# Kernel tuning notes

Hardware: AMD Instinct MI355X
Metric: run time of the kernel (lower is better)

The kernel has to match this reference:

```python
import jax, jax.numpy as jnp
import numpy as np

B, L, D_MODEL = 2, 2048, 1024
D_INNER, D_STATE, DT_RANK, D_CONV = 2048, 16, 64, 4
EPS = 1e-5


def setup_inputs() -> dict:
    key = jax.random.key(0)
    ks = jax.random.split(key, 12)
    s = lambda fan: 1.0 / np.sqrt(fan)
    return {
        "x": jax.random.normal(ks[0], (B, L, D_MODEL), jnp.float32),
        "norm_w": jnp.ones((D_MODEL,), jnp.float32),
        "W_in": jax.random.normal(ks[1], (2 * D_INNER, D_MODEL), jnp.float32) * s(D_MODEL),
        "W_conv": jax.random.normal(ks[2], (D_INNER, D_CONV), jnp.float32) * s(D_CONV),
        "b_conv": jnp.zeros((D_INNER,), jnp.float32),
        "W_xproj": jax.random.normal(ks[3], (DT_RANK + 2 * D_STATE, D_INNER), jnp.float32) * s(D_INNER),
        "W_dt": jax.random.normal(ks[4], (D_INNER, DT_RANK), jnp.float32) * s(DT_RANK),
        "b_dt": jax.random.normal(ks[5], (D_INNER,), jnp.float32) * 0.1,
        # A initialized as log(1..d_state) per channel (standard Mamba S4D-real init)
        "A_log": jnp.log(jnp.broadcast_to(jnp.arange(1, D_STATE + 1, dtype=jnp.float32), (D_INNER, D_STATE))),
        "D": jnp.ones((D_INNER,), jnp.float32),
        "W_out": jax.random.normal(ks[6], (D_MODEL, D_INNER), jnp.float32) * s(D_INNER),
    }


def _mamba_residual(x, norm_w, W_in, W_conv, b_conv, W_xproj, W_dt, b_dt, A_log, D, W_out):
    # RMSNorm
    xn = x * jax.lax.rsqrt(jnp.mean(x * x, axis=-1, keepdims=True) + EPS) * norm_w
    # in_proj -> split into u (ssm branch) and z (gate)
    xz = jnp.einsum("bld,ed->ble", xn, W_in)            # [b, l, 2*d_inner]
    u, z = jnp.split(xz, 2, axis=-1)                     # each [b, l, d_inner]
    # depthwise causal conv1d over time
    u_t = jnp.transpose(u, (0, 2, 1))                    # [b, d_inner, l]
    u_c = jax.lax.conv_general_dilated(
        u_t, W_conv[:, None, :], window_strides=(1,),
        padding=[(D_CONV - 1, 0)], feature_group_count=D_INNER,
        dimension_numbers=("NCH", "OIH", "NCH"))
    u_c = jax.nn.silu(u_c + b_conv[None, :, None])       # [b, d_inner, l]
    u = jnp.transpose(u_c, (0, 2, 1))                    # [b, l, d_inner]
    # x_proj -> (dt, B, C)
    x_dbl = jnp.einsum("bld,ed->ble", u, W_xproj)        # [b, l, dt_rank+2n]
    dt, Bm, Cm = jnp.split(x_dbl, [DT_RANK, DT_RANK + D_STATE], axis=-1)
    dt = jax.nn.softplus(jnp.einsum("blr,dr->bld", dt, W_dt) + b_dt)  # [b, l, d_inner]
    A = -jnp.exp(A_log)                                  # [d_inner, n]

    # selective scan over time
    def step(h, ins):
        dt_t, B_t, C_t, u_t = ins                        # [b,d],[b,n],[b,n],[b,d]
        dA = jnp.exp(dt_t[..., None] * A)                # [b, d, n]
        h = dA * h + (dt_t * u_t)[..., None] * B_t[:, None, :]
        y = jnp.einsum("bdn,bn->bd", h, C_t)
        return h, y

    h0 = jnp.zeros((x.shape[0], D_INNER, D_STATE), x.dtype)
    ins = (jnp.transpose(dt, (1, 0, 2)), jnp.transpose(Bm, (1, 0, 2)),
           jnp.transpose(Cm, (1, 0, 2)), jnp.transpose(u, (1, 0, 2)))
    _, ys = jax.lax.scan(step, h0, ins)                  # [l, b, d_inner]
    y = jnp.transpose(ys, (1, 0, 2)) + u * D             # [b, l, d_inner]
    y = y * jax.nn.silu(z)
    out = jnp.einsum("ble,de->bld", y, W_out)
    return out + x  # residual (block_mode 'residual'/'none')


def reference(x, norm_w, W_in, W_conv, b_conv, W_xproj, W_dt, b_dt, A_log, D, W_out):
    return _mamba_residual(x, norm_w, W_in, W_conv, b_conv, W_xproj, W_dt, b_dt, A_log, D, W_out)
```

## Files before the change

### kernel.cpp

```cpp
#include <hip/hip_runtime.h>

typedef unsigned short u16;
typedef unsigned int u32;
typedef short bf16x8 __attribute__((ext_vector_type(8)));
typedef float f32x4 __attribute__((ext_vector_type(4)));

static constexpr int LS = 2048;
static constexpr int DM = 1024;
static constexpr int DI = 2048;
static constexpr int DSn = 16;
static constexpr int DTRk = 64;
static constexpr int MR = 4096;
static constexpr int NCH = 64;
static constexpr int CL = LS / NCH;
static constexpr float L2E = 1.44269504f;

#define DEV __device__ __forceinline__

DEV u16 f2bf(float f) {
  u32 u = __float_as_uint(f);
  u32 r = (u + 0x7FFF + ((u >> 16) & 1)) >> 16;
  return (u16)r;
}
DEV float bf2f(u16 h) { return __uint_as_float(((u32)h) << 16); }

DEV void gload16(const u16* g, u16* l) {
  __builtin_amdgcn_global_load_lds((const __attribute__((address_space(1))) u32*)g,
                                   (__attribute__((address_space(3))) u32*)l, 16, 0, 0);
}

DEV void bar() { asm volatile("s_barrier" ::: "memory"); }

#define CALC_POWERS(dst, basev)                                              \
  do {                                                                       \
    const float e1_ = (basev);                                               \
    const float e2_ = e1_ * e1_, e3_ = e2_ * e1_, e4_ = e2_ * e2_;           \
    const float e5_ = e4_ * e1_, e6_ = e4_ * e2_, e7_ = e4_ * e3_,           \
                e8_ = e4_ * e4_;                                             \
    dst[0] = e1_; dst[1] = e2_; dst[2] = e3_; dst[3] = e4_;                  \
    dst[4] = e5_; dst[5] = e6_; dst[6] = e7_; dst[7] = e8_;                  \
    dst[8] = e8_ * e1_;  dst[9] = e8_ * e2_;  dst[10] = e8_ * e3_;           \
    dst[11] = e8_ * e4_; dst[12] = e8_ * e5_; dst[13] = e8_ * e6_;           \
    dst[14] = e8_ * e7_; dst[15] = e8_ * e8_;                                \
  } while (0)

__global__ __launch_bounds__(256) void cvt_weights(const float* __restrict__ W_in,
                                                   const float* __restrict__ W_out,
                                                   const float* __restrict__ W_dt,
                                                   const float* __restrict__ W_xp,
                                                   u16* __restrict__ Win_b,
                                                   u16* __restrict__ Wout_b,
                                                   u16* __restrict__ Wdt_b,
                                                   u16* __restrict__ Wxp_b) {
  const int N0 = 4096 * 1024;
  const int N1 = N0 + 1024 * 2048;
  const int N2 = N1 + 2048 * 64;
  const int N3 = N2 + 128 * 2048;
  int i = blockIdx.x * 256 + threadIdx.x;
  const int stride = gridDim.x * 256;
  for (; i < N3; i += stride) {
    if (i < N0) {
      Win_b[i] = f2bf(W_in[i]);
    } else if (i < N1) {
      const int j = i - N0; Wout_b[j] = f2bf(W_out[j]);
    } else if (i < N2) {
      const int j = i - N1; Wdt_b[j] = f2bf(W_dt[j]);
    } else {
      const int j = i - N2; const int r = j >> 11, c = j & 2047;
      Wxp_b[j] = (r < 96) ? f2bf(W_xp[r * 2048 + c]) : (u16)0;
    }
  }
}

__global__ __launch_bounds__(256) void rmsnorm_kernel(const float* __restrict__ x,
                                                      const float* __restrict__ w,
                                                      u16* __restrict__ xn) {
  const int row = blockIdx.x;
  const int tid = threadIdx.x;
  const float4 v = reinterpret_cast<const float4*>(x + (size_t)row * DM)[tid];
  float ss = v.x * v.x + v.y * v.y + v.z * v.z + v.w * v.w;
#pragma unroll
  for (int o = 32; o; o >>= 1) ss += __shfl_xor(ss, o);
  __shared__ float red[4];
  if ((tid & 63) == 0) red[tid >> 6] = ss;
  __syncthreads();
  const float tot = red[0] + red[1] + red[2] + red[3];
  const float scale = rsqrtf(tot * (1.0f / DM) + 1e-5f);
  const float4 wv = reinterpret_cast<const float4*>(w)[tid];
  ushort4 o4;
  o4.x = f2bf(v.x * scale * wv.x);
  o4.y = f2bf(v.y * scale * wv.y);
  o4.z = f2bf(v.z * scale * wv.z);
  o4.w = f2bf(v.w * scale * wv.w);
  *reinterpret_cast<ushort4*>(&xn[(size_t)row * DM + tid * 4]) = o4;
}

template <int EPI>
__global__ __launch_bounds__(512, 4) void gemm128n256(const u16* __restrict__ A,
                                                      const u16* __restrict__ Bw,
                                                      int M, int N, int K, int Klen,
                                                      u16* __restrict__ outB,
                                                      float* __restrict__ outF) {
  __shared__ __align__(16) u16 SL[2 * 12288];
  const int tid = threadIdx.x;
  const int lane = tid & 63;
  const int wid = tid >> 6;
  const int wr = wid >> 2;
  const int wc = wid & 3;
  const int lrow = lane & 15;
  const int kq = lane >> 4;

  const int nwg = gridDim.x * gridDim.y;
  int wg = blockIdx.y * gridDim.x + blockIdx.x;
  wg = (wg & 7) * (nwg >> 3) + (wg >> 3);
  const int bn = (wg % gridDim.x) * 256;
  const int bm = (wg / gridDim.x) * 128;
  const int koff = blockIdx.z * Klen;

  const int nt = Klen >> 5;

  f32x4 acc[4][4] = {};
  bf16x8 a[4], b[4];

  const int srA = tid >> 2;
  const int slA = (tid & 3) ^ ((srA >> 1) & 3);
  const int srB0 = tid >> 2, srB1 = 128 + (tid >> 2);
  const int slB0 = (tid & 3) ^ ((srB0 >> 1) & 3);
  const int slB1 = (tid & 3) ^ ((srB1 >> 1) & 3);

#define STAGE_TILE(ktile, sup)                                                          \
  do {                                                                                  \
    const int k0_ = koff + (ktile) * 32;                                                \
    gload16(A + (size_t)(bm + srA) * K + k0_ + slA * 8, &SL[(sup) + tid * 8]);          \
    gload16(Bw + (size_t)(bn + srB0) * K + k0_ + slB0 * 8, &SL[(sup) + 4096 + tid * 8]);\
    gload16(Bw + (size_t)(bn + srB1) * K + k0_ + slB1 * 8, &SL[(sup) + 8192 + tid * 8]);\
  } while (0)

  STAGE_TILE(0, 0);
  asm volatile("s_waitcnt vmcnt(0)" ::: "memory");
  bar();

  for (int t = 0; t < nt; ++t) {
    const int cs = (t & 1) * 12288;
    const int ns = ((t + 1) & 1) * 12288;
    if (t + 1 < nt) STAGE_TILE(t + 1, ns);
#pragma unroll
    for (int m = 0; m < 4; ++m) {
      const int row = wr * 64 + m * 16 + lrow;
      a[m] = *reinterpret_cast<const bf16x8*>(
          &SL[cs + row * 32 + (kq ^ ((row >> 1) & 3)) * 8]);
    }
#pragma unroll
    for (int n = 0; n < 4; ++n) {
      const int row = wc * 64 + n * 16 + lrow;
      b[n] = *reinterpret_cast<const bf16x8*>(
          &SL[cs + 4096 + row * 32 + (kq ^ ((row >> 1) & 3)) * 8]);
    }
    __builtin_amdgcn_s_setprio(1);
#pragma unroll
    for (int m = 0; m < 4; ++m)
#pragma unroll
      for (int n = 0; n < 4; ++n)
        acc[m][n] = __builtin_amdgcn_mfma_f32_16x16x32_bf16(a[m], b[n], acc[m][n], 0, 0, 0);
    __builtin_amdgcn_s_setprio(0);
    if (t + 1 < nt) {
      asm volatile("s_waitcnt vmcnt(0)" ::: "memory");
      bar();
    }
  }
#undef STAGE_TILE

  if (EPI == 0) {
#pragma unroll
    for (int m = 0; m < 4; ++m)
#pragma unroll
      for (int n = 0; n < 4; ++n) {
        const int col = bn + wc * 64 + n * 16 + lrow;
#pragma unroll
        for (int rr = 0; rr < 4; ++rr) {
          const int row = bm + wr * 64 + m * 16 + kq * 4 + rr;
          outB[(size_t)row * N + col] = f2bf(acc[m][n][rr]);
        }
      }
  } else {
    float* dstF = outF + (size_t)blockIdx.z * MR * N;
#pragma unroll
    for (int m = 0; m < 4; ++m)
#pragma unroll
      for (int n = 0; n < 4; ++n) {
        const int col = bn + wc * 64 + n * 16 + lrow;
#pragma unroll
        for (int rr = 0; rr < 4; ++rr) {
          const int row = bm + wr * 64 + m * 16 + kq * 4 + rr;
          dstF[(size_t)row * N + col] = acc[m][n][rr];
        }
      }
  }
}

__global__ __launch_bounds__(256) void outproj_reduce4(const float* __restrict__ p,
                                                       const float* __restrict__ x,
                                                       float* __restrict__ out) {
  const int id = blockIdx.x * 256 + threadIdx.x;
  float4 o = reinterpret_cast<const float4*>(x)[id];
#pragma unroll
  for (int s = 0; s < 4; ++s) {
    const float4 a = reinterpret_cast<const float4*>(p + (size_t)s * MR * 1024)[id];
    o.x += a.x; o.y += a.y; o.z += a.z; o.w += a.w;
  }
  reinterpret_cast<float4*>(out)[id] = o;
}

__global__ __launch_bounds__(256) void gemm_dt(const u16* __restrict__ A,
                                               const u16* __restrict__ Bw,
                                               int M, int N, int K,
                                               u16* __restrict__ outB,
                                               const float* __restrict__ aux) {
  __shared__ __align__(16) u16 As[128 * 32];
  __shared__ __align__(16) u16 Bs[128 * 32];
  const int tid = threadIdx.x;
  const int lane = tid & 63;
  const int wid = tid >> 6;
  const int wr = wid >> 1, wc = wid & 1;
  const int nwg = gridDim.x * gridDim.y;
  int wg = blockIdx.y * gridDim.x + blockIdx.x;
  wg = (wg & 7) * (nwg >> 3) + (wg >> 3);
  const int bn = (wg % gridDim.x) * 128;
  const int bm = (wg / gridDim.x) * 128;
  const int r0 = tid >> 2;
  const int c0 = (tid & 3) * 8;
  const int lrow = lane & 15, kq = lane >> 4;

  f32x4 acc[4][4] = {};

  const u16* Ab = A + (size_t)bm * K;
  const u16* Bb = Bw + (size_t)bn * K;

  for (int k0 = 0; k0 < K; k0 += 32) {
    gload16(Ab + (size_t)r0 * K + k0 + c0, &As[r0 * 32 + c0]);
    gload16(Ab + (size_t)(r0 + 64) * K + k0 + c0, &As[(r0 + 64) * 32 + c0]);
    gload16(Bb + (size_t)r0 * K + k0 + c0, &Bs[r0 * 32 + c0]);
    gload16(Bb + (size_t)(r0 + 64) * K + k0 + c0, &Bs[(r0 + 64) * 32 + c0]);
    __syncthreads();
    bf16x8 af[4], bfr[4];
#pragma unroll
    for (int m = 0; m < 4; ++m)
      af[m] = *reinterpret_cast<const bf16x8*>(&As[(wr * 64 + m * 16 + lrow) * 32 + kq * 8]);
#pragma unroll
    for (int n = 0; n < 4; ++n)
      bfr[n] = *reinterpret_cast<const bf16x8*>(&Bs[(wc * 64 + n * 16 + lrow) * 32 + kq * 8]);
#pragma unroll
    for (int m = 0; m < 4; ++m)
#pragma unroll
      for (int n = 0; n < 4; ++n)
        acc[m][n] = __builtin_amdgcn_mfma_f32_16x16x32_bf16(af[m], bfr[n], acc[m][n], 0, 0, 0);
    __syncthreads();
  }

#pragma unroll
  for (int m = 0; m < 4; ++m) {
#pragma unroll
    for (int n = 0; n < 4; ++n) {
      const int col = bn + wc * 64 + n * 16 + lrow;
#pragma unroll
      for (int r = 0; r < 4; ++r) {
        const int row = bm + wr * 64 + m * 16 + kq * 4 + r;
        const float xv = acc[m][n][r] + aux[col];
        const float sp = fmaxf(xv, 0.f) + log1pf(__expf(-fabsf(xv)));
        outB[(size_t)row * N + col] = f2bf(sp);
      }
    }
  }
}

__global__ __launch_bounds__(256) void gemm_xproj_splitk(const u16* __restrict__ A,
                                                         const u16* __restrict__ Bw,
                                                         float* __restrict__ p0,
                                                         float* __restrict__ p1) {
  __shared__ __align__(16) u16 As[128 * 32];
  __shared__ __align__(16) u16 Bs[128 * 32];
  const int tid = threadIdx.x;
  const int lane = tid & 63;
  const int wid = tid >> 6;
  const int wr = wid >> 1, wc = wid & 1;
  const int kp = blockIdx.x;
  const int bm = blockIdx.y * 128;
  const int koff = kp * 256;
  const int r0 = tid >> 2;
  const int c0 = (tid & 3) * 8;
  const int lrow = lane & 15, kq = lane >> 4;

  f32x4 acc[4][4] = {};
  const u16* Ab = A + (size_t)bm * DI + koff;
  const u16* Bb = Bw + koff;

  for (int k0 = 0; k0 < 256; k0 += 32) {
    gload16(Ab + (size_t)r0 * DI + k0 + c0, &As[r0 * 32 + c0]);
    gload16(Ab + (size_t)(r0 + 64) * DI + k0 + c0, &As[(r0 + 64) * 32 + c0]);
    gload16(Bb + (size_t)r0 * DI + k0 + c0, &Bs[r0 * 32 + c0]);
    gload16(Bb + (size_t)(r0 + 64) * DI + k0 + c0, &Bs[(r0 + 64) * 32 + c0]);
    __syncthreads();
    bf16x8 af[4], bfr[4];
#pragma unroll
    for (int m = 0; m < 4; ++m)
      af[m] = *reinterpret_cast<const bf16x8*>(&As[(wr * 64 + m * 16 + lrow) * 32 + kq * 8]);
#pragma unroll
    for (int n = 0; n < 4; ++n)
      bfr[n] = *reinterpret_cast<const bf16x8*>(&Bs[(wc * 64 + n * 16 + lrow) * 32 + kq * 8]);
#pragma unroll
    for (int m = 0; m < 4; ++m)
#pragma unroll
      for (int n = 0; n < 4; ++n)
        acc[m][n] = __builtin_amdgcn_mfma_f32_16x16x32_bf16(af[m], bfr[n], acc[m][n], 0, 0, 0);
    __syncthreads();
  }

  float* dst = (kp < 4 ? p0 : p1) + (size_t)(kp & 3) * MR * 128;
#pragma unroll
  for (int m = 0; m < 4; ++m)
#pragma unroll
    for (int n = 0; n < 4; ++n) {
      const int col = wc * 64 + n * 16 + lrow;
#pragma unroll
      for (int r = 0; r < 4; ++r) {
        const int row = bm + wr * 64 + m * 16 + kq * 4 + r;
        dst[(size_t)row * 128 + col] = acc[m][n][r];
      }
    }
}

__global__ __launch_bounds__(256) void xproj_reduce(const float* __restrict__ p0,
                                                    const float* __restrict__ p1,
                                                    float* __restrict__ xdbl,
                                                    u16* __restrict__ dtr) {
  const int id = blockIdx.x * 256 + threadIdx.x;
  const int row = id >> 7, col = id & 127;
  float s = 0.f;
#pragma unroll
  for (int kp = 0; kp < 4; ++kp) s += p0[(size_t)kp * MR * 128 + id];
#pragma unroll
  for (int kp = 0; kp < 4; ++kp) s += p1[(size_t)kp * MR * 128 + id];
  if (col < 96) xdbl[(size_t)row * 96 + col] = s;
  if (col < 64) dtr[(size_t)row * 64 + col] = f2bf(s);
}

__global__ __launch_bounds__(256) void conv_silu_kernel(const u16* __restrict__ xz,
                                                        const float* __restrict__ Wc,
                                                        const float* __restrict__ bc,
                                                        u16* __restrict__ uc) {
  const int id = blockIdx.x * 256 + threadIdx.x;
  const int d8 = id & (DI / 8 - 1);
  const int t = (id >> 8) & (LS - 1);
  const int b = id >> 19;
  const int d0 = d8 * 8;
  const size_t rowb = (size_t)b * LS;
  bf16x8 r[4];
#pragma unroll
  for (int k = 0; k < 4; ++k) {
    const int tt = t - 3 + k;
    if (tt >= 0)
      r[k] = *reinterpret_cast<const bf16x8*>(&xz[(rowb + tt) * (2 * DI) + d0]);
    else
      r[k] = bf16x8{0, 0, 0, 0, 0, 0, 0, 0};
  }
  const float4 bc0 = *reinterpret_cast<const float4*>(&bc[d0]);
  const float4 bc1 = *reinterpret_cast<const float4*>(&bc[d0 + 4]);
  const float bcv[8] = {bc0.x, bc0.y, bc0.z, bc0.w, bc1.x, bc1.y, bc1.z, bc1.w};
  u16 o[8];
#pragma unroll
  for (int j = 0; j < 8; ++j) {
    const float4 w = *reinterpret_cast<const float4*>(&Wc[(d0 + j) * 4]);
    float s = bcv[j];
    s += bf2f((u16)r[0][j]) * w.x;
    s += bf2f((u16)r[1][j]) * w.y;
    s += bf2f((u16)r[2][j]) * w.z;
    s += bf2f((u16)r[3][j]) * w.w;
    const float sl = s / (1.f + __expf(-s));
    o[j] = f2bf(sl);
  }
  *reinterpret_cast<bf16x8*>(&uc[(rowb + t) * DI + d0]) =
      *reinterpret_cast<const bf16x8*>(o);
}


__global__ __launch_bounds__(128, 4) void scan_phase1(const u16* __restrict__ dtb,
                                                      const float* __restrict__ xdbl,
                                                      const u16* __restrict__ uc,
                                                      const float* __restrict__ Alog,
                                                      float* __restrict__ P,
                                                      float* __restrict__ S) {
  __shared__ __align__(16) u16 s_dt[16 * 128];
  __shared__ __align__(16) u16 s_uc[16 * 128];
  __shared__ __align__(16) float s_b[16 * 16];
  const int tid = threadIdx.x;
  const int blk = blockIdx.x;
  const int d0 = (blk & 15) * 128;
  const int c = (blk >> 4) & (NCH - 1);
  const int b = blk >> 10;
  const int d = d0 + tid;
  const size_t tbase = (size_t)b * LS + c * CL;

  float Av[16];
  bool fastA = true;
#pragma unroll
  for (int j = 0; j < 16; j += 4) {
    const float4 Alv = *reinterpret_cast<const float4*>(&Alog[d * DSn + j]);
    Av[j + 0] = -__expf(Alv.x); Av[j + 1] = -__expf(Alv.y);
    Av[j + 2] = -__expf(Alv.z); Av[j + 3] = -__expf(Alv.w);
  }
#pragma unroll
  for (int j = 0; j < 16; ++j)
    fastA = fastA && (fabsf(Av[j] + (float)(j + 1)) < 1e-3f * (float)(j + 1));

  float h[16];
#pragma unroll
  for (int j = 0; j < 16; ++j) h[j] = 0.f;
  float sdt = 0.f;

  for (int w = 0; w < 2; ++w) {
    const size_t twb = tbase + w * 16;
#pragma unroll
    for (int j = 0; j < 2; ++j) {
      const int k = j * 128 + tid;
      const int row = k >> 4, col = (k & 15) * 8;
      gload16(dtb + (twb + row) * DI + d0 + col, &s_dt[row * 128 + col]);
      gload16(uc + (twb + row) * DI + d0 + col, &s_uc[row * 128 + col]);
    }
    if (tid < 64) {
      gload16((const u16*)(xdbl + (twb + (tid >> 2)) * 96 + DTRk + (tid & 3) * 4),
              (u16*)&s_b[tid * 4]);
    }
    __syncthreads();
    if (fastA) {
      for (int tr = 0; tr < 16; ++tr) {
        const float dtv = bf2f(s_dt[tr * 128 + tid]);
        const float uv = bf2f(s_uc[tr * 128 + tid]);
        const float du = dtv * uv;
        sdt += dtv;
        float dA[16];
        CALC_POWERS(dA, exp2f(-L2E * dtv));
        float Bf[16];
#pragma unroll
        for (int j = 0; j < 16; j += 4) {
          const float4 Bv = *reinterpret_cast<const float4*>(&s_b[tr * 16 + j]);
          Bf[j] = Bv.x; Bf[j + 1] = Bv.y; Bf[j + 2] = Bv.z; Bf[j + 3] = Bv.w;
        }
#pragma unroll
        for (int j = 0; j < 16; ++j) h[j] = dA[j] * h[j] + du * Bf[j];
      }
    } else {
      for (int tr = 0; tr < 16; ++tr) {
        const float dtv = bf2f(s_dt[tr * 128 + tid]);
        const float uv = bf2f(s_uc[tr * 128 + tid]);
        const float du = dtv * uv;
        sdt += dtv;
        float Bf[16];
#pragma unroll
        for (int j = 0; j < 16; j += 4) {
          const float4 Bv = *reinterpret_cast<const float4*>(&s_b[tr * 16 + j]);
          Bf[j] = Bv.x; Bf[j + 1] = Bv.y; Bf[j + 2] = Bv.z; Bf[j + 3] = Bv.w;
        }
#pragma unroll
        for (int j = 0; j < 16; ++j)
          h[j] = exp2f(dtv * Av[j] * L2E) * h[j] + du * Bf[j];
      }
    }
    __syncthreads();
  }

  const size_t oi = (((size_t)b * NCH + c) * DI + d) * DSn;
  float Pw[16];
  if (fastA) {
    CALC_POWERS(Pw, exp2f(-L2E * sdt));
  } else {
#pragma unroll
    for (int j = 0; j < 16; ++j) Pw[j] = exp2f(Av[j] * L2E * sdt);
  }
#pragma unroll
  for (int j = 0; j < 16; j += 4) {
    float4 Sv = {h[j], h[j + 1], h[j + 2], h[j + 3]};
    float4 Pv = {Pw[j], Pw[j + 1], Pw[j + 2], Pw[j + 3]};
    *reinterpret_cast<float4*>(&S[oi + j]) = Sv;
    *reinterpret_cast<float4*>(&P[oi + j]) = Pv;
  }
}

__global__ __launch_bounds__(256) void scan_phase2(const float* __restrict__ P,
                                                   float* __restrict__ S) {
  const int gid = blockIdx.x * 256 + threadIdx.x;
  const int ng = gid & 3;
  const int d = (gid >> 2) & (DI - 1);
  const int b = gid >> 13;
  float4 h = {0.f, 0.f, 0.f, 0.f};
  for (int cc = 0; cc < NCH; ++cc) {
    const size_t oi = (((size_t)b * NCH + cc) * DI + d) * DSn + ng * 4;
    const float4 Pv = *reinterpret_cast<const float4*>(&P[oi]);
    const float4 Sv = *reinterpret_cast<const float4*>(&S[oi]);
    *reinterpret_cast<float4*>(&S[oi]) = h;
    h.x = Sv.x + Pv.x * h.x;
    h.y = Sv.y + Pv.y * h.y;
    h.z = Sv.z + Pv.z * h.z;
    h.w = Sv.w + Pv.w * h.w;
  }
}

__global__ __launch_bounds__(128, 4) void scan_phase3(const u16* __restrict__ dtb,
                                                      const float* __restrict__ xdbl,
                                                      const u16* __restrict__ uc,
                                                      const u16* __restrict__ xz,
                                                      const float* __restrict__ Alog,
                                                      const float* __restrict__ Dp,
                                                      const float* __restrict__ Hin,
                                                      u16* __restrict__ yb) {
  __shared__ __align__(16) u16 s_dt[16 * 128];
  __shared__ __align__(16) u16 s_uc[16 * 128];
  __shared__ __align__(16) u16 s_z[16 * 128];
  __shared__ __align__(16) float s_bc[16 * 32];
  const int tid = threadIdx.x;
  const int blk = blockIdx.x;
  const int d0 = (blk & 15) * 128;
  const int c = (blk >> 4) & (NCH - 1);
  const int b = blk >> 10;
  const int d = d0 + tid;
  const size_t tbase = (size_t)b * LS + c * CL;

  float Av[16];
  bool fastA = true;
#pragma unroll
  for (int j = 0; j < 16; j += 4) {
    const float4 Alv = *reinterpret_cast<const float4*>(&Alog[d * DSn + j]);
    Av[j + 0] = -__expf(Alv.x); Av[j + 1] = -__expf(Alv.y);
    Av[j + 2] = -__expf(Alv.z); Av[j + 3] = -__expf(Alv.w);
  }
#pragma unroll
  for (int j = 0; j < 16; ++j)
    fastA = fastA && (fabsf(Av[j] + (float)(j + 1)) < 1e-3f * (float)(j + 1));

  const float Dd = Dp[d];
  const size_t oi = (((size_t)b * NCH + c) * DI + d) * DSn;
  float h[16];
#pragma unroll
  for (int j = 0; j < 16; j += 4) {
    const float4 hv = *reinterpret_cast<const float4*>(&Hin[oi + j]);
    h[j] = hv.x; h[j + 1] = hv.y; h[j + 2] = hv.z; h[j + 3] = hv.w;
  }

  for (int w = 0; w < 2; ++w) {
    const size_t twb = tbase + w * 16;
#pragma unroll
    for (int j = 0; j < 2; ++j) {
      const int k = j * 128 + tid;
      const int row = k >> 4, col = (k & 15) * 8;
      gload16(dtb + (twb + row) * DI + d0 + col, &s_dt[row * 128 + col]);
      gload16(uc + (twb + row) * DI + d0 + col, &s_uc[row * 128 + col]);
      gload16(xz + (twb + row) * (2 * DI) + DI + d0 + col, &s_z[row * 128 + col]);
    }
    {
      gload16((const u16*)(xdbl + (twb + (tid >> 3)) * 96 + DTRk + (tid & 7) * 4),
              (u16*)&s_bc[tid * 4]);
    }
    __syncthreads();
#define P3_STEP(DA_STMT)                                                        \
    for (int tr = 0; tr < 16; ++tr) {                                           \
      const float dtv = bf2f(s_dt[tr * 128 + tid]);                             \
      const float uv = bf2f(s_uc[tr * 128 + tid]);                              \
      const float du = dtv * uv;                                                \
      float dA[16];                                                             \
      DA_STMT;                                                                  \
      float Bf[16], Cf[16];                                                     \
      _Pragma("unroll")                                                         \
      for (int j = 0; j < 16; j += 4) {                                         \
        const float4 Bv = *reinterpret_cast<const float4*>(&s_bc[tr * 32 + j]); \
        const float4 Cv = *reinterpret_cast<const float4*>(&s_bc[tr * 32 + 16 + j]); \
        Bf[j] = Bv.x; Bf[j + 1] = Bv.y; Bf[j + 2] = Bv.z; Bf[j + 3] = Bv.w;     \
        Cf[j] = Cv.x; Cf[j + 1] = Cv.y; Cf[j + 2] = Cv.z; Cf[j + 3] = Cv.w;     \
      }                                                                         \
      _Pragma("unroll")                                                         \
      for (int j = 0; j < 16; ++j) h[j] = dA[j] * h[j] + du * Bf[j];            \
      float y0 = 0.f, y1 = 0.f, y2 = 0.f, y3 = 0.f;                             \
      _Pragma("unroll")                                                         \
      for (int j = 0; j < 16; j += 4) {                                         \
        y0 += h[j] * Cf[j];                                                     \
        y1 += h[j + 1] * Cf[j + 1];                                             \
        y2 += h[j + 2] * Cf[j + 2];                                             \
        y3 += h[j + 3] * Cf[j + 3];                                             \
      }                                                                         \
      const float y = (y0 + y1) + (y2 + y3) + uv * Dd;                          \
      const float z = bf2f(s_z[tr * 128 + tid]);                                \
      const float sz = z / (1.f + __expf(-z));                                  \
      yb[(twb + tr) * DI + d] = f2bf(y * sz);                                   \
    }
    if (fastA) {
      P3_STEP(CALC_POWERS(dA, exp2f(-L2E * dtv)));
    } else {
      P3_STEP({ _Pragma("unroll") for (int j = 0; j < 16; ++j) dA[j] = exp2f(dtv * Av[j] * L2E); });
    }
#undef P3_STEP
    __syncthreads();
  }
}

extern "C" void kernel_launch(void* const* d_in, const int* in_sizes, int n_in,
                              void* d_out, int out_size, void* d_ws, size_t ws_size,
                              hipStream_t stream) {
  (void)in_sizes; (void)n_in; (void)out_size; (void)ws_size;
  const float* x      = (const float*)d_in[0];
  const float* norm_w = (const float*)d_in[1];
  const float* W_in   = (const float*)d_in[2];
  const float* W_conv = (const float*)d_in[3];
  const float* b_conv = (const float*)d_in[4];
  const float* W_xp   = (const float*)d_in[5];
  const float* W_dt   = (const float*)d_in[6];
  const float* b_dt   = (const float*)d_in[7];
  const float* A_log  = (const float*)d_in[8];
  const float* Dvec   = (const float*)d_in[9];
  const float* W_out  = (const float*)d_in[10];
  float* out = (float*)d_out;

  char* ws = (char*)d_ws;
  size_t off = 0;
  auto alloc = [&](size_t bytes) -> void* {
    void* p = ws + off;
    off += (bytes + 255) & ~(size_t)255;
    return p;
  };
  u16* Win_b  = (u16*)alloc((size_t)4096 * 1024 * 2);
  u16* Wout_b = (u16*)alloc((size_t)1024 * 2048 * 2);
  u16* Wxp_b  = (u16*)alloc((size_t)128 * 2048 * 2);
  u16* Wdt_b  = (u16*)alloc((size_t)2048 * 64 * 2);
  u16* xn_b   = (u16*)alloc((size_t)MR * DM * 2);
  u16* xz_b   = (u16*)alloc((size_t)MR * 2 * DI * 2);
  u16* uc_b   = (u16*)alloc((size_t)MR * DI * 2);
  float* xdbl = (float*)alloc((size_t)MR * 96 * 4);
  u16* dtr_b  = (u16*)alloc((size_t)MR * 64 * 2);
  u16* dtf_b  = (u16*)alloc((size_t)MR * DI * 2);
  u16* y_b    = (u16*)alloc((size_t)MR * DI * 2);
  float* Sbuf = (float*)alloc((size_t)2 * NCH * DI * DSn * 4);
  float* part0 = (float*)Win_b;
  float* part1 = (float*)xn_b;
  float* Pbuf = (float*)y_b;
  float* opart = (float*)xz_b;

  cvt_weights<<<2048, 256, 0, stream>>>(W_in, W_out, W_dt, W_xp,
                                        Win_b, Wout_b, Wdt_b, Wxp_b);

  rmsnorm_kernel<<<MR, 256, 0, stream>>>(x, norm_w, xn_b);

  gemm128n256<0><<<dim3(16, 32, 1), 512, 0, stream>>>(xn_b, Win_b, MR, 4096, 1024, 1024,
                                                      xz_b, nullptr);
  conv_silu_kernel<<<4096, 256, 0, stream>>>(xz_b, W_conv, b_conv, uc_b);
  gemm_xproj_splitk<<<dim3(8, 32), 256, 0, stream>>>(uc_b, Wxp_b, part0, part1);
  xproj_reduce<<<2048, 256, 0, stream>>>(part0, part1, xdbl, dtr_b);
  gemm_dt<<<dim3(16, 32), 256, 0, stream>>>(dtr_b, Wdt_b, MR, 2048, 64, dtf_b, b_dt);
  scan_phase1<<<2048, 128, 0, stream>>>(dtf_b, xdbl, uc_b, A_log, Pbuf, Sbuf);
  scan_phase2<<<64, 256, 0, stream>>>(Pbuf, Sbuf);
  scan_phase3<<<2048, 128, 0, stream>>>(dtf_b, xdbl, uc_b, xz_b, A_log, Dvec,
                                        Sbuf, y_b);
  gemm128n256<1><<<dim3(4, 32, 4), 512, 0, stream>>>(y_b, Wout_b, MR, 1024, 2048, 512,
                                                     nullptr, opart);
  outproj_reduce4<<<4096, 256, 0, stream>>>(opart, x, out);
}
```

Measured before the change: 230.8 us.

## Fuse RMSNorm into weight conversion and recompute chunk decay in scan phase 2

```diff
diff --git a/kernel.cpp b/kernel.cpp
--- a/kernel.cpp
+++ b/kernel.cpp
@@ -44,19 +44,42 @@
     dst[14] = e8_ * e7_; dst[15] = e8_ * e8_;                                \
   } while (0)
 
-__global__ __launch_bounds__(256) void cvt_weights(const float* __restrict__ W_in,
-                                                   const float* __restrict__ W_out,
-                                                   const float* __restrict__ W_dt,
-                                                   const float* __restrict__ W_xp,
-                                                   u16* __restrict__ Win_b,
-                                                   u16* __restrict__ Wout_b,
-                                                   u16* __restrict__ Wdt_b,
-                                                   u16* __restrict__ Wxp_b) {
+__global__ __launch_bounds__(256) void cvt_norm(const float* __restrict__ x,
+                                                const float* __restrict__ w,
+                                                const float* __restrict__ W_in,
+                                                const float* __restrict__ W_out,
+                                                const float* __restrict__ W_dt,
+                                                const float* __restrict__ W_xp,
+                                                u16* __restrict__ xn,
+                                                u16* __restrict__ Win_b,
+                                                u16* __restrict__ Wout_b,
+                                                u16* __restrict__ Wdt_b,
+                                                u16* __restrict__ Wxp_b) {
+  const int row = blockIdx.x;
+  const int tid = threadIdx.x;
+  {
+    const float4 v = reinterpret_cast<const float4*>(x + (size_t)row * DM)[tid];
+    float ss = v.x * v.x + v.y * v.y + v.z * v.z + v.w * v.w;
+#pragma unroll
+    for (int o = 32; o; o >>= 1) ss += __shfl_xor(ss, o);
+    __shared__ float red[4];
+    if ((tid & 63) == 0) red[tid >> 6] = ss;
+    __syncthreads();
+    const float tot = red[0] + red[1] + red[2] + red[3];
+    const float scale = rsqrtf(tot * (1.0f / DM) + 1e-5f);
+    const float4 wv = reinterpret_cast<const float4*>(w)[tid];
+    ushort4 o4;
+    o4.x = f2bf(v.x * scale * wv.x);
+    o4.y = f2bf(v.y * scale * wv.y);
+    o4.z = f2bf(v.z * scale * wv.z);
+    o4.w = f2bf(v.w * scale * wv.w);
+    *reinterpret_cast<ushort4*>(&xn[(size_t)row * DM + tid * 4]) = o4;
+  }
   const int N0 = 4096 * 1024;
   const int N1 = N0 + 1024 * 2048;
   const int N2 = N1 + 2048 * 64;
   const int N3 = N2 + 128 * 2048;
-  int i = blockIdx.x * 256 + threadIdx.x;
+  int i = blockIdx.x * 256 + tid;
   const int stride = gridDim.x * 256;
   for (; i < N3; i += stride) {
     if (i < N0) {
@@ -70,29 +93,6 @@
       Wxp_b[j] = (r < 96) ? f2bf(W_xp[r * 2048 + c]) : (u16)0;
     }
   }
-}
-
-__global__ __launch_bounds__(256) void rmsnorm_kernel(const float* __restrict__ x,
-                                                      const float* __restrict__ w,
-                                                      u16* __restrict__ xn) {
-  const int row = blockIdx.x;
-  const int tid = threadIdx.x;
-  const float4 v = reinterpret_cast<const float4*>(x + (size_t)row * DM)[tid];
-  float ss = v.x * v.x + v.y * v.y + v.z * v.z + v.w * v.w;
-#pragma unroll
-  for (int o = 32; o; o >>= 1) ss += __shfl_xor(ss, o);
-  __shared__ float red[4];
-  if ((tid & 63) == 0) red[tid >> 6] = ss;
-  __syncthreads();
-  const float tot = red[0] + red[1] + red[2] + red[3];
-  const float scale = rsqrtf(tot * (1.0f / DM) + 1e-5f);
-  const float4 wv = reinterpret_cast<const float4*>(w)[tid];
-  ushort4 o4;
-  o4.x = f2bf(v.x * scale * wv.x);
-  o4.y = f2bf(v.y * scale * wv.y);
-  o4.z = f2bf(v.z * scale * wv.z);
-  o4.w = f2bf(v.w * scale * wv.w);
-  *reinterpret_cast<ushort4*>(&xn[(size_t)row * DM + tid * 4]) = o4;
 }
 
 template <int EPI>
@@ -387,7 +387,7 @@
                                                       const float* __restrict__ xdbl,
                                                       const u16* __restrict__ uc,
                                                       const float* __restrict__ Alog,
-                                                      float* __restrict__ P,
+                                                      float* __restrict__ sdtb,
                                                       float* __restrict__ S) {
   __shared__ __align__(16) u16 s_dt[16 * 128];
   __shared__ __align__(16) u16 s_uc[16 * 128];
@@ -469,32 +469,33 @@
   }
 
   const size_t oi = (((size_t)b * NCH + c) * DI + d) * DSn;
-  float Pw[16];
-  if (fastA) {
-    CALC_POWERS(Pw, exp2f(-L2E * sdt));
-  } else {
-#pragma unroll
-    for (int j = 0; j < 16; ++j) Pw[j] = exp2f(Av[j] * L2E * sdt);
-  }
 #pragma unroll
   for (int j = 0; j < 16; j += 4) {
     float4 Sv = {h[j], h[j + 1], h[j + 2], h[j + 3]};
-    float4 Pv = {Pw[j], Pw[j + 1], Pw[j + 2], Pw[j + 3]};
     *reinterpret_cast<float4*>(&S[oi + j]) = Sv;
-    *reinterpret_cast<float4*>(&P[oi + j]) = Pv;
-  }
-}
-
-__global__ __launch_bounds__(256) void scan_phase2(const float* __restrict__ P,
+  }
+  sdtb[((size_t)b * NCH + c) * DI + d] = sdt;
+}
+
+__global__ __launch_bounds__(256) void scan_phase2(const float* __restrict__ Alog,
+                                                   const float* __restrict__ sdtb,
                                                    float* __restrict__ S) {
   const int gid = blockIdx.x * 256 + threadIdx.x;
   const int ng = gid & 3;
   const int d = (gid >> 2) & (DI - 1);
   const int b = gid >> 13;
+  const float4 Alv = *reinterpret_cast<const float4*>(&Alog[d * DSn + ng * 4]);
+  const float Av[4] = {-__expf(Alv.x) * L2E, -__expf(Alv.y) * L2E,
+                       -__expf(Alv.z) * L2E, -__expf(Alv.w) * L2E};
   float4 h = {0.f, 0.f, 0.f, 0.f};
   for (int cc = 0; cc < NCH; ++cc) {
+    const float sdt = sdtb[((size_t)b * NCH + cc) * DI + d];
+    float4 Pv;
+    Pv.x = exp2f(Av[0] * sdt);
+    Pv.y = exp2f(Av[1] * sdt);
+    Pv.z = exp2f(Av[2] * sdt);
+    Pv.w = exp2f(Av[3] * sdt);
     const size_t oi = (((size_t)b * NCH + cc) * DI + d) * DSn + ng * 4;
-    const float4 Pv = *reinterpret_cast<const float4*>(&P[oi]);
     const float4 Sv = *reinterpret_cast<const float4*>(&S[oi]);
     *reinterpret_cast<float4*>(&S[oi]) = h;
     h.x = Sv.x + Pv.x * h.x;
@@ -638,13 +639,11 @@
   float* Sbuf = (float*)alloc((size_t)2 * NCH * DI * DSn * 4);
   float* part0 = (float*)Win_b;
   float* part1 = (float*)xn_b;
-  float* Pbuf = (float*)y_b;
+  float* sdtb = (float*)y_b;
   float* opart = (float*)xz_b;
 
-  cvt_weights<<<2048, 256, 0, stream>>>(W_in, W_out, W_dt, W_xp,
-                                        Win_b, Wout_b, Wdt_b, Wxp_b);
-
-  rmsnorm_kernel<<<MR, 256, 0, stream>>>(x, norm_w, xn_b);
+  cvt_norm<<<MR, 256, 0, stream>>>(x, norm_w, W_in, W_out, W_dt, W_xp,
+                                   xn_b, Win_b, Wout_b, Wdt_b, Wxp_b);
 
   gemm128n256<0><<<dim3(16, 32, 1), 512, 0, stream>>>(xn_b, Win_b, MR, 4096, 1024, 1024,
                                                       xz_b, nullptr);
@@ -652,8 +651,8 @@
   gemm_xproj_splitk<<<dim3(8, 32), 256, 0, stream>>>(uc_b, Wxp_b, part0, part1);
   xproj_reduce<<<2048, 256, 0, stream>>>(part0, part1, xdbl, dtr_b);
   gemm_dt<<<dim3(16, 32), 256, 0, stream>>>(dtr_b, Wdt_b, MR, 2048, 64, dtf_b, b_dt);
-  scan_phase1<<<2048, 128, 0, stream>>>(dtf_b, xdbl, uc_b, A_log, Pbuf, Sbuf);
-  scan_phase2<<<64, 256, 0, stream>>>(Pbuf, Sbuf);
+  scan_phase1<<<2048, 128, 0, stream>>>(dtf_b, xdbl, uc_b, A_log, sdtb, Sbuf);
+  scan_phase2<<<64, 256, 0, stream>>>(A_log, sdtb, Sbuf);
   scan_phase3<<<2048, 128, 0, stream>>>(dtf_b, xdbl, uc_b, xz_b, A_log, Dvec,
                                         Sbuf, y_b);
   gemm128n256<1><<<dim3(4, 32, 4), 512, 0, stream>>>(y_b, Wout_b, MR, 1024, 2048, 512,
```

Measured after the change: 226.8 us. About the same (-1.7%).
